# Performance work log

Hardware: AMD Instinct MI355X
Metric: run time of the kernel (lower is better)

## Reference

```python
import jax, jax.numpy as jnp
import numpy as np

CH = 128
GROUPS = 8
EPS = 1e-5

def group_norm(x, w, b):
    B, C, H, W = x.shape
    g = x.reshape(B, GROUPS, C // GROUPS, H, W)
    mean = g.mean(axis=(2, 3, 4), keepdims=True)
    var = g.var(axis=(2, 3, 4), keepdims=True)
    g = (g - mean) * jax.lax.rsqrt(var + EPS)
    g = g.reshape(B, C, H, W)
    return g * w[None, :, None, None] + b[None, :, None, None]

def setup_inputs() -> dict:
    key = jax.random.key(0)
    ks = jax.random.split(key, 7)
    C = CH
    x = jax.random.normal(ks[0], (8, C, 64, 64), dtype=jnp.float32)
    gn_w = jnp.ones((C,), dtype=jnp.float32)
    gn_b = jnp.zeros((C,), dtype=jnp.float32)
    s = 1.0 / np.sqrt(C)
    qkv_w = jax.random.normal(ks[1], (3 * C, C), dtype=jnp.float32) * s
    qkv_b = jax.random.normal(ks[2], (3 * C,), dtype=jnp.float32) * 0.01
    proj_w = jax.random.normal(ks[3], (C, C), dtype=jnp.float32) * s
    proj_b = jax.random.normal(ks[4], (C,), dtype=jnp.float32) * 0.01
    return {"x": x, "gn_w": gn_w, "gn_b": gn_b, "qkv_w": qkv_w,
            "qkv_b": qkv_b, "proj_w": proj_w, "proj_b": proj_b}

def reference(x, gn_w, gn_b, qkv_w, qkv_b, proj_w, proj_b):
    B, C, H, W = x.shape
    h = group_norm(x, gn_w, gn_b)
    # 1x1 conv == per-pixel matmul over channels
    qkv = jnp.einsum('bchw,oc->bohw', h, qkv_w) + qkv_b[None, :, None, None]
    q, k, v = jnp.split(qkv.reshape(B, 3 * C, H * W), 3, axis=1)  # each [B,C,N]
    scale = C ** (-0.5)
    attn = jax.nn.softmax(jnp.einsum('bci,bcj->bij', q * scale, k), axis=-1)
    out = jnp.einsum('bij,bcj->bci', attn, v).reshape(B, C, H, W)
    out = jnp.einsum('bchw,oc->bohw', out, proj_w) + proj_b[None, :, None, None]
    return x + out
```

## Files before the change

### kernel.cpp

```cpp
#include <hip/hip_runtime.h>
#include <stdint.h>


typedef __attribute__((ext_vector_type(8))) short short8;
typedef __attribute__((ext_vector_type(4))) float f32x4;
typedef __attribute__((ext_vector_type(16))) float f32x16;

#define MFMA_BF16(a, b, c) __builtin_amdgcn_mfma_f32_16x16x32_bf16((a), (b), (c), 0, 0, 0)
#define MFMA32(a, b, c) __builtin_amdgcn_mfma_f32_32x32x16_bf16((a), (b), (c), 0, 0, 0)
#define EXP2(x) __builtin_amdgcn_exp2f(x)

#define QSCALE 0.12751743f

__device__ __forceinline__ unsigned short f2bf(float f) {
    unsigned int u = __builtin_bit_cast(unsigned int, f);
    u += 0x7FFFu + ((u >> 16) & 1u);
    return (unsigned short)(u >> 16);
}
__device__ __forceinline__ float bf2f(unsigned int lo16) {
    return __builtin_bit_cast(float, lo16 << 16);
}
__device__ __forceinline__ short8 ldg8(const unsigned short* p) {
    return __builtin_bit_cast(short8, *(const uint4*)p);
}
__device__ __forceinline__ unsigned int cvtpk(float lo, float hi) {
    unsigned int r;
    asm("v_cvt_pk_bf16_f32 %0, %1, %2" : "=v"(r) : "v"(lo), "v"(hi));
    return r;
}
__device__ __forceinline__ void gload16(const void* g, void* l) {
    __builtin_amdgcn_global_load_lds(
        (__attribute__((address_space(1))) void*)g,
        (__attribute__((address_space(3))) void*)l, 16, 0, 0);
}

__global__ __launch_bounds__(256) void k_pre(const float* __restrict__ x,
                                             float* __restrict__ sums,
                                             const float* __restrict__ qkv_w,
                                             const float* __restrict__ proj_w,
                                             unsigned short* __restrict__ wq,
                                             unsigned short* __restrict__ wp) {
    if (blockIdx.x >= 1024) {
        int i = ((blockIdx.x - 1024) * 256 + threadIdx.x) * 4;
        const float* src; unsigned short* dst; int off;
        if (i < 49152) { src = qkv_w; dst = wq; off = i; }
        else           { src = proj_w; dst = wp; off = i - 49152; }
        float4 v = *(const float4*)(src + off);
        uint2 pk;
        pk.x = (unsigned int)f2bf(v.x) | ((unsigned int)f2bf(v.y) << 16);
        pk.y = (unsigned int)f2bf(v.z) | ((unsigned int)f2bf(v.w) << 16);
        *(uint2*)(dst + off) = pk;
        return;
    }
    int g     = blockIdx.x >> 4;
    int slice = blockIdx.x & 15;
    const float* p = x + (size_t)g * 65536 + slice * 4096;
    float s = 0.f, sq = 0.f;
#pragma unroll
    for (int i = 0; i < 4; ++i) {
        float4 v = *(const float4*)(p + threadIdx.x * 4 + i * 1024);
        s  += v.x + v.y + v.z + v.w;
        sq += v.x*v.x + v.y*v.y + v.z*v.z + v.w*v.w;
    }
#pragma unroll
    for (int m = 1; m < 64; m <<= 1) { s += __shfl_xor(s, m, 64); sq += __shfl_xor(sq, m, 64); }
    __shared__ float ss[4], ssq[4];
    int w = threadIdx.x >> 6;
    if ((threadIdx.x & 63) == 0) { ss[w] = s; ssq[w] = sq; }
    __syncthreads();
    if (threadIdx.x == 0) {
        sums[(g * 16 + slice) * 2]     = ss[0] + ss[1] + ss[2] + ss[3];
        sums[(g * 16 + slice) * 2 + 1] = ssq[0] + ssq[1] + ssq[2] + ssq[3];
    }
}

__global__ __launch_bounds__(256) void k_qkv(const float* __restrict__ x,
                                             const float* __restrict__ sums,
                                             const float* __restrict__ gn_w,
                                             const float* __restrict__ gn_b,
                                             const unsigned short* __restrict__ wq,
                                             const float* __restrict__ qkv_b,
                                             unsigned short* __restrict__ k_ws,
                                             unsigned short* __restrict__ v_ws) {
    __shared__ unsigned short h_lds[64][144];
    __shared__ float ms[8][2];
    const int tid  = threadIdx.x;
    const int b    = blockIdx.x >> 6;
    const int n0   = (blockIdx.x & 63) << 6;
    const int lane = tid & 63, wave = tid >> 6;
    const int l15  = lane & 15, q4 = lane >> 4;

    if (tid < 8) {
        float s = 0.f, q = 0.f;
        const float* sp = sums + (size_t)(b * 8 + tid) * 32;
#pragma unroll
        for (int i = 0; i < 16; ++i) { s += sp[i * 2]; q += sp[i * 2 + 1]; }
        float mean = s * (1.f / 65536.f);
        float var  = q * (1.f / 65536.f) - mean * mean;
        ms[tid][0] = mean;
        ms[tid][1] = rsqrtf(var + 1e-5f);
    }
    __syncthreads();

    {
        int cb = tid >> 4;
        int nn = (tid & 15) << 2;
#pragma unroll
        for (int k = 0; k < 8; ++k) {
            int c = cb + (k << 4);
            float4 v = *(const float4*)(x + ((size_t)(b * 128 + c) << 12) + n0 + nn);
            int g = c >> 4;
            float mean = ms[g][0];
            float rstd = ms[g][1];
            float ga = gn_w[c] * rstd;
            float be = gn_b[c] - mean * ga;
            h_lds[nn + 0][c] = f2bf(v.x * ga + be);
            h_lds[nn + 1][c] = f2bf(v.y * ga + be);
            h_lds[nn + 2][c] = f2bf(v.z * ga + be);
            h_lds[nn + 3][c] = f2bf(v.w * ga + be);
        }
    }
    __syncthreads();

    short8 bfrag[4][4];
#pragma unroll
    for (int nt = 0; nt < 4; ++nt)
#pragma unroll
        for (int ks = 0; ks < 4; ++ks)
            bfrag[nt][ks] = *(const short8*)&h_lds[nt * 16 + l15][ks * 32 + q4 * 8];
    __syncthreads();

    unsigned short* vstage = &h_lds[0][0];

#pragma unroll
    for (int ot = 0; ot < 4; ++ot) {
        int o0 = wave * 64 + ot * 16;
        short8 af[4];
#pragma unroll
        for (int ks = 0; ks < 4; ++ks)
            af[ks] = ldg8(wq + (size_t)(128 + o0 + l15) * 128 + ks * 32 + q4 * 8);

        if (o0 < 128) {
            float bias[4];
#pragma unroll
            for (int r = 0; r < 4; ++r) bias[r] = qkv_b[128 + o0 + q4 * 4 + r];
#pragma unroll
            for (int nt = 0; nt < 4; ++nt) {
                f32x4 acc = {0.f, 0.f, 0.f, 0.f};
#pragma unroll
                for (int ks = 0; ks < 4; ++ks)
                    acc = MFMA_BF16(af[ks], bfrag[nt][ks], acc);
                int n = n0 + nt * 16 + l15;
                unsigned int lo = (unsigned int)f2bf(acc[0] + bias[0]) |
                                  ((unsigned int)f2bf(acc[1] + bias[1]) << 16);
                unsigned int hi = (unsigned int)f2bf(acc[2] + bias[2]) |
                                  ((unsigned int)f2bf(acc[3] + bias[3]) << 16);
                uint2 pk; pk.x = lo; pk.y = hi;
                *(uint2*)&k_ws[((size_t)(b * 4096 + n) << 7) + o0 + q4 * 4] = pk;
            }
        } else {
            int c = o0 - 128 + l15;
            float vb = qkv_b[128 + o0 + l15];
#pragma unroll
            for (int nt = 0; nt < 4; ++nt) {
                f32x4 acc = {0.f, 0.f, 0.f, 0.f};
#pragma unroll
                for (int ks = 0; ks < 4; ++ks)
                    acc = MFMA_BF16(bfrag[nt][ks], af[ks], acc);
                unsigned int lo = (unsigned int)f2bf(acc[0] + vb) |
                                  ((unsigned int)f2bf(acc[1] + vb) << 16);
                unsigned int hi = (unsigned int)f2bf(acc[2] + vb) |
                                  ((unsigned int)f2bf(acc[3] + vb) << 16);
                uint2 pk; pk.x = lo; pk.y = hi;
                *(uint2*)&vstage[c * 72 + nt * 16 + q4 * 4] = pk;
            }
        }
    }
    __syncthreads();

    {
        int c = tid >> 1, hf = tid & 1;
        const unsigned short* src = vstage + c * 72 + hf * 32;
        unsigned short* dst = v_ws + ((size_t)(b * 128 + c) << 12) + n0 + hf * 32;
        uint4 a0 = *(const uint4*)(src + 0);
        uint4 a1 = *(const uint4*)(src + 8);
        uint4 a2 = *(const uint4*)(src + 16);
        uint4 a3 = *(const uint4*)(src + 24);
        *(uint4*)(dst + 0)  = a0;
        *(uint4*)(dst + 8)  = a1;
        *(uint4*)(dst + 16) = a2;
        *(uint4*)(dst + 24) = a3;
    }
}

__global__ __launch_bounds__(512, 2) void k_attn(const float* __restrict__ sums,
                                                 const float* __restrict__ gn_w,
                                                 const float* __restrict__ gn_b,
                                                 const unsigned short* __restrict__ wq,
                                                 const float* __restrict__ qkv_b,
                                                 const unsigned short* __restrict__ k_ws,
                                                 const unsigned short* __restrict__ v_ws,
                                                 const float* __restrict__ x,
                                                 const unsigned short* __restrict__ wp,
                                                 const float* __restrict__ proj_b,
                                                 float* __restrict__ out) {
    __shared__ unsigned short K0[64][128];
    __shared__ unsigned short K1[64][128];
    __shared__ unsigned short V0[128][64];
    __shared__ unsigned short V1[128][64];
    __shared__ unsigned short O_lds[128][136];
    __shared__ float Lp[256];
    __shared__ float ms[8][2];

    const int tid   = threadIdx.x;
    const int b     = blockIdx.x & 7;
    const int tile  = blockIdx.x >> 3;
    const int i0    = tile << 7;
    const int lane  = tid & 63, wave = tid >> 6;
    const int ih    = wave >> 1, jh = wave & 1;
    const int l31   = lane & 31, h = lane >> 5;
    const int irow  = ih * 32 + l31;

    if (tid < 8) {
        float s = 0.f, q = 0.f;
        const float* sp = sums + (size_t)(b * 8 + tid) * 32;
#pragma unroll
        for (int i = 0; i < 16; ++i) { s += sp[i * 2]; q += sp[i * 2 + 1]; }
        float mean = s * (1.f / 65536.f);
        float var  = q * (1.f / 65536.f) - mean * mean;
        ms[tid][0] = mean;
        ms[tid][1] = rsqrtf(var + 1e-5f);
    }
    __syncthreads();

    {
        int c = tid >> 2, qq = tid & 3;
        float mean = ms[c >> 4][0], rstd = ms[c >> 4][1];
        float ga = gn_w[c] * rstd;
        float be = gn_b[c] - mean * ga;
        const float* xp = x + ((size_t)(b * 128 + c) << 12) + i0 + qq * 32;
#pragma unroll
        for (int k = 0; k < 8; ++k) {
            float4 v = *(const float4*)(xp + k * 4);
            int il = qq * 32 + k * 4;
            O_lds[il + 0][c] = f2bf(v.x * ga + be);
            O_lds[il + 1][c] = f2bf(v.y * ga + be);
            O_lds[il + 2][c] = f2bf(v.z * ga + be);
            O_lds[il + 3][c] = f2bf(v.w * ga + be);
        }
    }
    __syncthreads();

    {
        const int l15 = lane & 15, q4 = lane >> 4;
        int o0q = wave * 16;
        short8 af[4];
#pragma unroll
        for (int ks = 0; ks < 4; ++ks)
            af[ks] = ldg8(wq + (size_t)(o0q + l15) * 128 + ks * 32 + q4 * 8);
        float qb[4];
#pragma unroll
        for (int r = 0; r < 4; ++r) qb[r] = qkv_b[o0q + q4 * 4 + r];
#pragma unroll
        for (int nt = 0; nt < 8; ++nt) {
            f32x4 qacc = {0.f, 0.f, 0.f, 0.f};
#pragma unroll
            for (int ks = 0; ks < 4; ++ks) {
                short8 bf = *(const short8*)&O_lds[nt * 16 + l15][ks * 32 + q4 * 8];
                qacc = MFMA_BF16(af[ks], bf, qacc);
            }
            unsigned int lo = (unsigned int)f2bf((qacc[0] + qb[0]) * QSCALE) |
                              ((unsigned int)f2bf((qacc[1] + qb[1]) * QSCALE) << 16);
            unsigned int hi = (unsigned int)f2bf((qacc[2] + qb[2]) * QSCALE) |
                              ((unsigned int)f2bf((qacc[3] + qb[3]) * QSCALE) << 16);
            uint2 pk; pk.x = lo; pk.y = hi;
            unsigned short* qrow = (nt < 4) ? &K0[nt * 16 + l15][0]
                                            : &K1[(nt - 4) * 16 + l15][0];
            *(uint2*)(qrow + o0q + q4 * 4) = pk;
        }
    }
    __syncthreads();

    short8 qf[8];
    {
        const unsigned short* qrow = (ih < 2) ? &K0[irow][0] : &K1[irow - 64][0];
#pragma unroll
        for (int ks = 0; ks < 8; ++ks)
            qf[ks] = *(const short8*)(qrow + ks * 16 + h * 8);
    }
    __syncthreads();

    f32x16 acc[4];
#pragma unroll
    for (int ct = 0; ct < 4; ++ct)
#pragma unroll
        for (int e = 0; e < 16; ++e) acc[ct][e] = 0.f;
    float l_run = 0.f;

    const unsigned short* kbase = k_ws + ((size_t)b << 19);
    int ksrc[2];
#pragma unroll
    for (int q = 0; q < 2; ++q) {
        int c   = q * 512 + tid;
        int row = c >> 4;
        ksrc[q] = row * 16 + ((c & 15) ^ (row & 15));
    }
    const unsigned short* vlane = v_ws + ((size_t)b << 19) +
        ((size_t)(tid >> 3) << 12) +
        ((((tid & 7) ^ ((tid >> 3) & 7) ^ wave)) << 3);

#define STAGE(T, KD, VD)                                                              \
  do {                                                                                \
    _Pragma("unroll")                                                                 \
    for (int q = 0; q < 2; ++q)                                                       \
      gload16(kbase + (size_t)(T) * 8192 + ksrc[q] * 8,                               \
              (char*)(&KD[0][0]) + q * 8192 + wave * 1024);                           \
    _Pragma("unroll")                                                                 \
    for (int q = 0; q < 2; ++q)                                                       \
      gload16(vlane + (size_t)q * 262144 + (T) * 64,                                  \
              (char*)(&VD[0][0]) + q * 8192 + wave * 1024);                           \
  } while (0)

#define BAR_A()                                                                       \
  do {                                                                                \
    asm volatile("s_waitcnt vmcnt(0)" ::: "memory");                                  \
    __builtin_amdgcn_s_barrier();                                                     \
    __builtin_amdgcn_sched_barrier(0);                                                \
  } while (0)

    const int krow = jh * 32 + l31;
    const int ksw  = l31 & 15;
    const int vk   = (l31 & 7) ^ (l31 >> 3);

    STAGE(0, K0, V0);

#define ATTN_ITER(IT, KR, VR, KP, VP)                                                 \
  do {                                                                                \
    BAR_A();                          \
    if ((IT) < 63) STAGE((IT) + 1, KP, VP);           \
    f32x16 s;        \
    _Pragma("unroll")                                                                 \
    for (int e = 0; e < 16; ++e) s[e] = 0.f;                                          \
    _Pragma("unroll")                                                                 \
    for (int ks = 0; ks < 8; ++ks) {                                                  \
      short8 kf = *(const short8*)&KR[krow][((ks * 2 + h) ^ ksw) << 3];               \
      s = MFMA32(kf, qf[ks], s);                                                      \
    }                                                                                 \
    float pvv[16];                         \
    _Pragma("unroll")                                                                 \
    for (int e = 0; e < 16; ++e) pvv[e] = EXP2(fminf(s[e], 30.f));                    \
    l_run += (((pvv[0] + pvv[1]) + (pvv[2] + pvv[3])) +                               \
              ((pvv[4] + pvv[5]) + (pvv[6] + pvv[7]))) +                              \
             (((pvv[8] + pvv[9]) + (pvv[10] + pvv[11])) +                             \
              ((pvv[12] + pvv[13]) + (pvv[14] + pvv[15])));                           \
    short8 paf[2];     \
    _Pragma("unroll")                                                                 \
    for (int ks = 0; ks < 2; ++ks) {                                                  \
      const float* pp = pvv + ks * 8;                                                 \
      unsigned int Wa = cvtpk(pp[0], pp[1]);                                          \
      unsigned int Wc = cvtpk(pp[2], pp[3]);                                          \
      unsigned int Wb = cvtpk(pp[4], pp[5]);                                          \
      unsigned int Wd = cvtpk(pp[6], pp[7]);                                          \
      auto r1 = __builtin_amdgcn_permlane32_swap(Wa, Wb, false, false);               \
      auto r2 = __builtin_amdgcn_permlane32_swap(Wc, Wd, false, false);               \
      uint4 aw; aw.x = r1[0]; aw.y = r2[0]; aw.z = r1[1]; aw.w = r2[1];               \
      paf[ks] = __builtin_bit_cast(short8, aw);              \
    }                                                                                 \
    _Pragma("unroll")                                                                 \
    for (int ks = 0; ks < 2; ++ks)                                                    \
      _Pragma("unroll")                                                               \
      for (int ct = 0; ct < 4; ++ct) {                                                \
        short8 vf = *(const short8*)&VR[ct * 32 + l31]                                \
            [((jh * 4 + ks * 2 + h) ^ vk ^ ((ct & 1) << 2)) << 3];                    \
        acc[ct] = MFMA32(paf[ks], vf, acc[ct]);                                       \
      }                                                                               \
  } while (0)

    for (int ib = 0; ib < 32; ++ib) {
        int it = ib * 2;
        ATTN_ITER(it,     K0, V0, K1, V1);
        ATTN_ITER(it + 1, K1, V1, K0, V0);
    }
#undef ATTN_ITER
#undef STAGE
#undef BAR_A

    __syncthreads();
    float l2 = l_run + __shfl_xor(l_run, 32);
    if (h == 0) Lp[jh * 128 + irow] = l2;
    float* ObLow  = (ih < 2) ? (float*)&K0[0][0] : (float*)&K1[0][0];
    float* ObHigh = (ih < 2) ? (float*)&V0[0][0] : (float*)&V1[0][0];
    const int vbase = (ih & 1) * 32;
    if (jh) {
#pragma unroll
        for (int cc = 0; cc < 2; ++cc)
#pragma unroll
            for (int r = 0; r < 16; ++r) {
                int il = (r & 3) + ((r >> 2) << 3) + (h << 2);
                ObLow[(vbase + il) * 64 + cc * 32 + l31] = (cc == 0) ? acc[0][r] : acc[1][r];
            }
    } else {
#pragma unroll
        for (int cc = 0; cc < 2; ++cc)
#pragma unroll
            for (int r = 0; r < 16; ++r) {
                int il = (r & 3) + ((r >> 2) << 3) + (h << 2);
                ObHigh[(vbase + il) * 64 + cc * 32 + l31] = (cc == 0) ? acc[2][r] : acc[3][r];
            }
    }
    __syncthreads();
    {
        float rl[16];
#pragma unroll
        for (int r = 0; r < 16; ++r) {
            int il = (r & 3) + ((r >> 2) << 3) + (h << 2);
            rl[r] = 1.0f / (Lp[ih * 32 + il] + Lp[128 + ih * 32 + il]);
        }
        if (jh) {
#pragma unroll
            for (int cc = 0; cc < 2; ++cc)
#pragma unroll
                for (int r = 0; r < 16; ++r) {
                    int il = (r & 3) + ((r >> 2) << 3) + (h << 2);
                    float own = (cc == 0) ? acc[2][r] : acc[3][r];
                    float v = own + ObHigh[(vbase + il) * 64 + cc * 32 + l31];
                    O_lds[ih * 32 + il][64 + cc * 32 + l31] = f2bf(v * rl[r]);
                }
        } else {
#pragma unroll
            for (int cc = 0; cc < 2; ++cc)
#pragma unroll
                for (int r = 0; r < 16; ++r) {
                    int il = (r & 3) + ((r >> 2) << 3) + (h << 2);
                    float own = (cc == 0) ? acc[0][r] : acc[1][r];
                    float v = own + ObLow[(vbase + il) * 64 + cc * 32 + l31];
                    O_lds[ih * 32 + il][cc * 32 + l31] = f2bf(v * rl[r]);
                }
        }
    }
    __syncthreads();

    {
        const int l15 = lane & 15, q4 = lane >> 4;
        int o0 = wave * 16;
        short8 af[4];
#pragma unroll
        for (int ks = 0; ks < 4; ++ks)
            af[ks] = ldg8(wp + (size_t)(o0 + l15) * 128 + ks * 32 + q4 * 8);
        float pb[4];
#pragma unroll
        for (int r = 0; r < 4; ++r) pb[r] = proj_b[o0 + q4 * 4 + r];

#pragma unroll
        for (int nt = 0; nt < 8; ++nt) {
            f32x4 pacc = {0.f, 0.f, 0.f, 0.f};
#pragma unroll
            for (int ks = 0; ks < 4; ++ks) {
                short8 bf = *(const short8*)&O_lds[nt * 16 + l15][ks * 32 + q4 * 8];
                pacc = MFMA_BF16(af[ks], bf, pacc);
            }
#pragma unroll
            for (int r = 0; r < 4; ++r) {
                size_t idx = ((size_t)(b * 128 + o0 + q4 * 4 + r) << 12) +
                             i0 + nt * 16 + l15;
                out[idx] = x[idx] + pacc[r] + pb[r];
            }
        }
    }
}

extern "C" void kernel_launch(void* const* d_in, const int* in_sizes, int n_in,
                              void* d_out, int out_size, void* d_ws, size_t ws_size,
                              hipStream_t stream) {
    const float* x      = (const float*)d_in[0];
    const float* gn_w   = (const float*)d_in[1];
    const float* gn_b   = (const float*)d_in[2];
    const float* qkv_w  = (const float*)d_in[3];
    const float* qkv_b  = (const float*)d_in[4];
    const float* proj_w = (const float*)d_in[5];
    const float* proj_b = (const float*)d_in[6];
    float* out = (float*)d_out;

    char* ws = (char*)d_ws;
    float* sums           = (float*)ws;
    unsigned short* wq    = (unsigned short*)(ws + 16384);
    unsigned short* wp    = (unsigned short*)(ws + 16384 + 98304);
    unsigned short* k_ws  = (unsigned short*)(ws + ((size_t)1 << 20));
    unsigned short* v_ws  = (unsigned short*)(ws + ((size_t)9 << 20));

    k_pre<<<1088, 256, 0, stream>>>(x, sums, qkv_w, proj_w, wq, wp);
    k_qkv<<<512, 256, 0, stream>>>(x, sums, gn_w, gn_b, wq, qkv_b, k_ws, v_ws);
    k_attn<<<256, 512, 0, stream>>>(sums, gn_w, gn_b, wq, qkv_b, k_ws, v_ws,
                                    x, wp, proj_b, out);
}
```

Before: 175.4 us.

## Fuse all three stages into one cooperative kernel with grid-wide syncs

Merges the stats/weight-conversion, QKV projection and attention kernels into a single cooperative kernel of 256 blocks that uses grid.sync between phases. Each block computes partial group-norm sums for its own 128-pixel tile, then after a grid barrier normalizes, projects Q into LDS and writes its K/V tile to the workspace. A second grid barrier precedes attention. This removes two kernel launches and the redundant re-read of x for the stats, at the cost of grid-wide barriers and the occupancy limits that cooperative launch imposes.

```diff
diff --git a/kernel.cpp b/kernel.cpp
--- a/kernel.cpp
+++ b/kernel.cpp
@@ -1,6 +1,9 @@
 #include <hip/hip_runtime.h>
+#include <hip/hip_cooperative_groups.h>
 #include <stdint.h>
 
+
+namespace cg = cooperative_groups;
 
 typedef __attribute__((ext_vector_type(8))) short short8;
 typedef __attribute__((ext_vector_type(4))) float f32x4;
@@ -17,9 +20,6 @@
     u += 0x7FFFu + ((u >> 16) & 1u);
     return (unsigned short)(u >> 16);
 }
-__device__ __forceinline__ float bf2f(unsigned int lo16) {
-    return __builtin_bit_cast(float, lo16 << 16);
-}
 __device__ __forceinline__ short8 ldg8(const unsigned short* p) {
     return __builtin_bit_cast(short8, *(const uint4*)p);
 }
@@ -34,67 +34,74 @@
         (__attribute__((address_space(3))) void*)l, 16, 0, 0);
 }
 
-__global__ __launch_bounds__(256) void k_pre(const float* __restrict__ x,
-                                             float* __restrict__ sums,
-                                             const float* __restrict__ qkv_w,
-                                             const float* __restrict__ proj_w,
-                                             unsigned short* __restrict__ wq,
-                                             unsigned short* __restrict__ wp) {
-    if (blockIdx.x >= 1024) {
-        int i = ((blockIdx.x - 1024) * 256 + threadIdx.x) * 4;
+__global__ __launch_bounds__(512, 2) void k_fused(const float* __restrict__ x,
+                                                  float* __restrict__ sums,
+                                                  const float* __restrict__ qkv_w_raw,
+                                                  const float* __restrict__ proj_w_raw,
+                                                  unsigned short* __restrict__ wq,
+                                                  unsigned short* __restrict__ wp,
+                                                  const float* __restrict__ gn_w,
+                                                  const float* __restrict__ gn_b,
+                                                  const float* __restrict__ qkv_b,
+                                                  unsigned short* __restrict__ k_ws,
+                                                  unsigned short* __restrict__ v_ws,
+                                                  const float* __restrict__ proj_b,
+                                                  float* __restrict__ out) {
+    __shared__ unsigned short K0[64][128];
+    __shared__ unsigned short K1[64][128];
+    __shared__ unsigned short V0[128][64];
+    __shared__ unsigned short V1[128][64];
+    __shared__ unsigned short O_lds[128][136];
+    __shared__ float Lp[256];
+    __shared__ float ms[8][2];
+
+    const int tid   = threadIdx.x;
+    const int b     = blockIdx.x & 7;
+    const int tile  = blockIdx.x >> 3;
+    const int i0    = tile << 7;
+    const int lane  = tid & 63, wave = tid >> 6;
+    const int ih    = wave >> 1, jh = wave & 1;
+    const int l31   = lane & 31, h = lane >> 5;
+    const int irow  = ih * 32 + l31;
+    const int l15   = lane & 15, q4 = lane >> 4;
+
+    cg::grid_group grid = cg::this_grid();
+
+    if (tid < 64) {
+        int i = (blockIdx.x * 64 + tid) * 4;
         const float* src; unsigned short* dst; int off;
-        if (i < 49152) { src = qkv_w; dst = wq; off = i; }
-        else           { src = proj_w; dst = wp; off = i - 49152; }
+        if (i < 49152) { src = qkv_w_raw; dst = wq; off = i; }
+        else           { src = proj_w_raw; dst = wp; off = i - 49152; }
         float4 v = *(const float4*)(src + off);
         uint2 pk;
         pk.x = (unsigned int)f2bf(v.x) | ((unsigned int)f2bf(v.y) << 16);
         pk.y = (unsigned int)f2bf(v.z) | ((unsigned int)f2bf(v.w) << 16);
         *(uint2*)(dst + off) = pk;
-        return;
-    }
-    int g     = blockIdx.x >> 4;
-    int slice = blockIdx.x & 15;
-    const float* p = x + (size_t)g * 65536 + slice * 4096;
-    float s = 0.f, sq = 0.f;
-#pragma unroll
-    for (int i = 0; i < 4; ++i) {
-        float4 v = *(const float4*)(p + threadIdx.x * 4 + i * 1024);
-        s  += v.x + v.y + v.z + v.w;
-        sq += v.x*v.x + v.y*v.y + v.z*v.z + v.w*v.w;
-    }
-#pragma unroll
-    for (int m = 1; m < 64; m <<= 1) { s += __shfl_xor(s, m, 64); sq += __shfl_xor(sq, m, 64); }
-    __shared__ float ss[4], ssq[4];
-    int w = threadIdx.x >> 6;
-    if ((threadIdx.x & 63) == 0) { ss[w] = s; ssq[w] = sq; }
-    __syncthreads();
-    if (threadIdx.x == 0) {
-        sums[(g * 16 + slice) * 2]     = ss[0] + ss[1] + ss[2] + ss[3];
-        sums[(g * 16 + slice) * 2 + 1] = ssq[0] + ssq[1] + ssq[2] + ssq[3];
-    }
-}
-
-__global__ __launch_bounds__(256) void k_qkv(const float* __restrict__ x,
-                                             const float* __restrict__ sums,
-                                             const float* __restrict__ gn_w,
-                                             const float* __restrict__ gn_b,
-                                             const unsigned short* __restrict__ wq,
-                                             const float* __restrict__ qkv_b,
-                                             unsigned short* __restrict__ k_ws,
-                                             unsigned short* __restrict__ v_ws) {
-    __shared__ unsigned short h_lds[64][144];
-    __shared__ float ms[8][2];
-    const int tid  = threadIdx.x;
-    const int b    = blockIdx.x >> 6;
-    const int n0   = (blockIdx.x & 63) << 6;
-    const int lane = tid & 63, wave = tid >> 6;
-    const int l15  = lane & 15, q4 = lane >> 4;
+    }
+    {
+        int c = tid >> 2, qq = tid & 3;
+        const float* xp = x + ((size_t)(b * 128 + c) << 12) + i0 + qq * 32;
+        float s = 0.f, sq = 0.f;
+#pragma unroll
+        for (int k = 0; k < 8; ++k) {
+            float4 v = *(const float4*)(xp + k * 4);
+            s  += v.x + v.y + v.z + v.w;
+            sq += v.x*v.x + v.y*v.y + v.z*v.z + v.w*v.w;
+        }
+#pragma unroll
+        for (int m = 1; m < 64; m <<= 1) { s += __shfl_xor(s, m, 64); sq += __shfl_xor(sq, m, 64); }
+        if (lane == 0) {
+            sums[((b * 8 + wave) * 32 + tile) * 2]     = s;
+            sums[((b * 8 + wave) * 32 + tile) * 2 + 1] = sq;
+        }
+    }
+    grid.sync();
 
     if (tid < 8) {
         float s = 0.f, q = 0.f;
-        const float* sp = sums + (size_t)(b * 8 + tid) * 32;
-#pragma unroll
-        for (int i = 0; i < 16; ++i) { s += sp[i * 2]; q += sp[i * 2 + 1]; }
+        const float* sp = sums + (size_t)((b * 8 + tid) * 32) * 2;
+#pragma unroll
+        for (int i = 0; i < 32; ++i) { s += sp[i * 2]; q += sp[i * 2 + 1]; }
         float mean = s * (1.f / 65536.f);
         float var  = q * (1.f / 65536.f) - mean * mean;
         ms[tid][0] = mean;
@@ -103,85 +110,109 @@
     __syncthreads();
 
     {
-        int cb = tid >> 4;
-        int nn = (tid & 15) << 2;
+        int c = tid >> 2, qq = tid & 3;
+        float mean = ms[c >> 4][0], rstd = ms[c >> 4][1];
+        float ga = gn_w[c] * rstd;
+        float be = gn_b[c] - mean * ga;
+        const float* xp = x + ((size_t)(b * 128 + c) << 12) + i0 + qq * 32;
 #pragma unroll
         for (int k = 0; k < 8; ++k) {
-            int c = cb + (k << 4);
-            float4 v = *(const float4*)(x + ((size_t)(b * 128 + c) << 12) + n0 + nn);
-            int g = c >> 4;
-            float mean = ms[g][0];
-            float rstd = ms[g][1];
-            float ga = gn_w[c] * rstd;
-            float be = gn_b[c] - mean * ga;
-            h_lds[nn + 0][c] = f2bf(v.x * ga + be);
-            h_lds[nn + 1][c] = f2bf(v.y * ga + be);
-            h_lds[nn + 2][c] = f2bf(v.z * ga + be);
-            h_lds[nn + 3][c] = f2bf(v.w * ga + be);
-        }
-    }
-    __syncthreads();
-
-    short8 bfrag[4][4];
-#pragma unroll
-    for (int nt = 0; nt < 4; ++nt)
+            float4 v = *(const float4*)(xp + k * 4);
+            int il = qq * 32 + k * 4;
+            O_lds[il + 0][c] = f2bf(v.x * ga + be);
+            O_lds[il + 1][c] = f2bf(v.y * ga + be);
+            O_lds[il + 2][c] = f2bf(v.z * ga + be);
+            O_lds[il + 3][c] = f2bf(v.w * ga + be);
+        }
+    }
+    __syncthreads();
+
+    {
+        int o0q = wave * 16;
+        short8 af[4];
 #pragma unroll
         for (int ks = 0; ks < 4; ++ks)
-            bfrag[nt][ks] = *(const short8*)&h_lds[nt * 16 + l15][ks * 32 + q4 * 8];
-    __syncthreads();
-
-    unsigned short* vstage = &h_lds[0][0];
-
-#pragma unroll
-    for (int ot = 0; ot < 4; ++ot) {
-        int o0 = wave * 64 + ot * 16;
+            af[ks] = ldg8(wq + (size_t)(o0q + l15) * 128 + ks * 32 + q4 * 8);
+        float qb[4];
+#pragma unroll
+        for (int r = 0; r < 4; ++r) qb[r] = qkv_b[o0q + q4 * 4 + r];
+#pragma unroll
+        for (int nt = 0; nt < 8; ++nt) {
+            f32x4 qacc = {0.f, 0.f, 0.f, 0.f};
+#pragma unroll
+            for (int ks = 0; ks < 4; ++ks) {
+                short8 bf = *(const short8*)&O_lds[nt * 16 + l15][ks * 32 + q4 * 8];
+                qacc = MFMA_BF16(af[ks], bf, qacc);
+            }
+            unsigned int lo = (unsigned int)f2bf((qacc[0] + qb[0]) * QSCALE) |
+                              ((unsigned int)f2bf((qacc[1] + qb[1]) * QSCALE) << 16);
+            unsigned int hi = (unsigned int)f2bf((qacc[2] + qb[2]) * QSCALE) |
+                              ((unsigned int)f2bf((qacc[3] + qb[3]) * QSCALE) << 16);
+            uint2 pk; pk.x = lo; pk.y = hi;
+            unsigned short* qrow = (nt < 4) ? &K0[nt * 16 + l15][0]
+                                            : &K1[(nt - 4) * 16 + l15][0];
+            *(uint2*)(qrow + o0q + q4 * 4) = pk;
+        }
+    }
+    {
+        int o0 = wave * 16;
         short8 af[4];
 #pragma unroll
         for (int ks = 0; ks < 4; ++ks)
             af[ks] = ldg8(wq + (size_t)(128 + o0 + l15) * 128 + ks * 32 + q4 * 8);
-
-        if (o0 < 128) {
-            float bias[4];
-#pragma unroll
-            for (int r = 0; r < 4; ++r) bias[r] = qkv_b[128 + o0 + q4 * 4 + r];
-#pragma unroll
-            for (int nt = 0; nt < 4; ++nt) {
-                f32x4 acc = {0.f, 0.f, 0.f, 0.f};
-#pragma unroll
-                for (int ks = 0; ks < 4; ++ks)
-                    acc = MFMA_BF16(af[ks], bfrag[nt][ks], acc);
-                int n = n0 + nt * 16 + l15;
-                unsigned int lo = (unsigned int)f2bf(acc[0] + bias[0]) |
-                                  ((unsigned int)f2bf(acc[1] + bias[1]) << 16);
-                unsigned int hi = (unsigned int)f2bf(acc[2] + bias[2]) |
-                                  ((unsigned int)f2bf(acc[3] + bias[3]) << 16);
-                uint2 pk; pk.x = lo; pk.y = hi;
-                *(uint2*)&k_ws[((size_t)(b * 4096 + n) << 7) + o0 + q4 * 4] = pk;
-            }
-        } else {
-            int c = o0 - 128 + l15;
-            float vb = qkv_b[128 + o0 + l15];
-#pragma unroll
-            for (int nt = 0; nt < 4; ++nt) {
-                f32x4 acc = {0.f, 0.f, 0.f, 0.f};
-#pragma unroll
-                for (int ks = 0; ks < 4; ++ks)
-                    acc = MFMA_BF16(bfrag[nt][ks], af[ks], acc);
-                unsigned int lo = (unsigned int)f2bf(acc[0] + vb) |
-                                  ((unsigned int)f2bf(acc[1] + vb) << 16);
-                unsigned int hi = (unsigned int)f2bf(acc[2] + vb) |
-                                  ((unsigned int)f2bf(acc[3] + vb) << 16);
-                uint2 pk; pk.x = lo; pk.y = hi;
-                *(uint2*)&vstage[c * 72 + nt * 16 + q4 * 4] = pk;
-            }
-        }
-    }
-    __syncthreads();
-
-    {
-        int c = tid >> 1, hf = tid & 1;
-        const unsigned short* src = vstage + c * 72 + hf * 32;
-        unsigned short* dst = v_ws + ((size_t)(b * 128 + c) << 12) + n0 + hf * 32;
+        float bias[4];
+#pragma unroll
+        for (int r = 0; r < 4; ++r) bias[r] = qkv_b[128 + o0 + q4 * 4 + r];
+#pragma unroll
+        for (int nt = 0; nt < 8; ++nt) {
+            f32x4 acc = {0.f, 0.f, 0.f, 0.f};
+#pragma unroll
+            for (int ks = 0; ks < 4; ++ks) {
+                short8 bf = *(const short8*)&O_lds[nt * 16 + l15][ks * 32 + q4 * 8];
+                acc = MFMA_BF16(af[ks], bf, acc);
+            }
+            int n = i0 + nt * 16 + l15;
+            unsigned int lo = (unsigned int)f2bf(acc[0] + bias[0]) |
+                              ((unsigned int)f2bf(acc[1] + bias[1]) << 16);
+            unsigned int hi = (unsigned int)f2bf(acc[2] + bias[2]) |
+                              ((unsigned int)f2bf(acc[3] + bias[3]) << 16);
+            uint2 pk; pk.x = lo; pk.y = hi;
+            *(uint2*)&k_ws[((size_t)(b * 4096 + n) << 7) + o0 + q4 * 4] = pk;
+        }
+    }
+    {
+        int c = wave * 16 + l15;
+        short8 af[4];
+#pragma unroll
+        for (int ks = 0; ks < 4; ++ks)
+            af[ks] = ldg8(wq + (size_t)(256 + wave * 16 + l15) * 128 + ks * 32 + q4 * 8);
+        float vb = qkv_b[256 + wave * 16 + l15];
+        unsigned short* vrow = ((wave < 4) ? (unsigned short*)&V0[0][0]
+                                           : (unsigned short*)&V1[0][0]) + (c & 63) * 128;
+#pragma unroll
+        for (int nt = 0; nt < 8; ++nt) {
+            f32x4 acc = {0.f, 0.f, 0.f, 0.f};
+#pragma unroll
+            for (int ks = 0; ks < 4; ++ks) {
+                short8 bf = *(const short8*)&O_lds[nt * 16 + l15][ks * 32 + q4 * 8];
+                acc = MFMA_BF16(bf, af[ks], acc);
+            }
+            unsigned int lo = (unsigned int)f2bf(acc[0] + vb) |
+                              ((unsigned int)f2bf(acc[1] + vb) << 16);
+            unsigned int hi = (unsigned int)f2bf(acc[2] + vb) |
+                              ((unsigned int)f2bf(acc[3] + vb) << 16);
+            uint2 pk; pk.x = lo; pk.y = hi;
+            *(uint2*)&vrow[nt * 16 + q4 * 4] = pk;
+        }
+    }
+    __syncthreads();
+
+    {
+        int c = tid >> 2, qq = tid & 3;
+        const unsigned short* src = ((c < 64) ? (const unsigned short*)&V0[0][0]
+                                              : (const unsigned short*)&V1[0][0]) +
+                                    (c & 63) * 128 + qq * 32;
+        unsigned short* dst = v_ws + ((size_t)(b * 128 + c) << 12) + i0 + qq * 32;
         uint4 a0 = *(const uint4*)(src + 0);
         uint4 a1 = *(const uint4*)(src + 8);
         uint4 a2 = *(const uint4*)(src + 16);
@@ -191,96 +222,6 @@
         *(uint4*)(dst + 16) = a2;
         *(uint4*)(dst + 24) = a3;
     }
-}
-
-__global__ __launch_bounds__(512, 2) void k_attn(const float* __restrict__ sums,
-                                                 const float* __restrict__ gn_w,
-                                                 const float* __restrict__ gn_b,
-                                                 const unsigned short* __restrict__ wq,
-                                                 const float* __restrict__ qkv_b,
-                                                 const unsigned short* __restrict__ k_ws,
-                                                 const unsigned short* __restrict__ v_ws,
-                                                 const float* __restrict__ x,
-                                                 const unsigned short* __restrict__ wp,
-                                                 const float* __restrict__ proj_b,
-                                                 float* __restrict__ out) {
-    __shared__ unsigned short K0[64][128];
-    __shared__ unsigned short K1[64][128];
-    __shared__ unsigned short V0[128][64];
-    __shared__ unsigned short V1[128][64];
-    __shared__ unsigned short O_lds[128][136];
-    __shared__ float Lp[256];
-    __shared__ float ms[8][2];
-
-    const int tid   = threadIdx.x;
-    const int b     = blockIdx.x & 7;
-    const int tile  = blockIdx.x >> 3;
-    const int i0    = tile << 7;
-    const int lane  = tid & 63, wave = tid >> 6;
-    const int ih    = wave >> 1, jh = wave & 1;
-    const int l31   = lane & 31, h = lane >> 5;
-    const int irow  = ih * 32 + l31;
-
-    if (tid < 8) {
-        float s = 0.f, q = 0.f;
-        const float* sp = sums + (size_t)(b * 8 + tid) * 32;
-#pragma unroll
-        for (int i = 0; i < 16; ++i) { s += sp[i * 2]; q += sp[i * 2 + 1]; }
-        float mean = s * (1.f / 65536.f);
-        float var  = q * (1.f / 65536.f) - mean * mean;
-        ms[tid][0] = mean;
-        ms[tid][1] = rsqrtf(var + 1e-5f);
-    }
-    __syncthreads();
-
-    {
-        int c = tid >> 2, qq = tid & 3;
-        float mean = ms[c >> 4][0], rstd = ms[c >> 4][1];
-        float ga = gn_w[c] * rstd;
-        float be = gn_b[c] - mean * ga;
-        const float* xp = x + ((size_t)(b * 128 + c) << 12) + i0 + qq * 32;
-#pragma unroll
-        for (int k = 0; k < 8; ++k) {
-            float4 v = *(const float4*)(xp + k * 4);
-            int il = qq * 32 + k * 4;
-            O_lds[il + 0][c] = f2bf(v.x * ga + be);
-            O_lds[il + 1][c] = f2bf(v.y * ga + be);
-            O_lds[il + 2][c] = f2bf(v.z * ga + be);
-            O_lds[il + 3][c] = f2bf(v.w * ga + be);
-        }
-    }
-    __syncthreads();
-
-    {
-        const int l15 = lane & 15, q4 = lane >> 4;
-        int o0q = wave * 16;
-        short8 af[4];
-#pragma unroll
-        for (int ks = 0; ks < 4; ++ks)
-            af[ks] = ldg8(wq + (size_t)(o0q + l15) * 128 + ks * 32 + q4 * 8);
-        float qb[4];
-#pragma unroll
-        for (int r = 0; r < 4; ++r) qb[r] = qkv_b[o0q + q4 * 4 + r];
-#pragma unroll
-        for (int nt = 0; nt < 8; ++nt) {
-            f32x4 qacc = {0.f, 0.f, 0.f, 0.f};
-#pragma unroll
-            for (int ks = 0; ks < 4; ++ks) {
-                short8 bf = *(const short8*)&O_lds[nt * 16 + l15][ks * 32 + q4 * 8];
-                qacc = MFMA_BF16(af[ks], bf, qacc);
-            }
-            unsigned int lo = (unsigned int)f2bf((qacc[0] + qb[0]) * QSCALE) |
-                              ((unsigned int)f2bf((qacc[1] + qb[1]) * QSCALE) << 16);
-            unsigned int hi = (unsigned int)f2bf((qacc[2] + qb[2]) * QSCALE) |
-                              ((unsigned int)f2bf((qacc[3] + qb[3]) * QSCALE) << 16);
-            uint2 pk; pk.x = lo; pk.y = hi;
-            unsigned short* qrow = (nt < 4) ? &K0[nt * 16 + l15][0]
-                                            : &K1[(nt - 4) * 16 + l15][0];
-            *(uint2*)(qrow + o0q + q4 * 4) = pk;
-        }
-    }
-    __syncthreads();
-
     short8 qf[8];
     {
         const unsigned short* qrow = (ih < 2) ? &K0[irow][0] : &K1[irow - 64][0];
@@ -289,6 +230,7 @@
             qf[ks] = *(const short8*)(qrow + ks * 16 + h * 8);
     }
     __syncthreads();
+    grid.sync();
 
     f32x16 acc[4];
 #pragma unroll
@@ -336,9 +278,9 @@
 
 #define ATTN_ITER(IT, KR, VR, KP, VP)                                                 \
   do {                                                                                \
-    BAR_A();                          \
-    if ((IT) < 63) STAGE((IT) + 1, KP, VP);           \
-    f32x16 s;        \
+    BAR_A();                                                                          \
+    if ((IT) < 63) STAGE((IT) + 1, KP, VP);                                           \
+    f32x16 s;                                                                         \
     _Pragma("unroll")                                                                 \
     for (int e = 0; e < 16; ++e) s[e] = 0.f;                                          \
     _Pragma("unroll")                                                                 \
@@ -346,14 +288,14 @@
       short8 kf = *(const short8*)&KR[krow][((ks * 2 + h) ^ ksw) << 3];               \
       s = MFMA32(kf, qf[ks], s);                                                      \
     }                                                                                 \
-    float pvv[16];                         \
+    float pvv[16];                                                                    \
     _Pragma("unroll")                                                                 \
     for (int e = 0; e < 16; ++e) pvv[e] = EXP2(fminf(s[e], 30.f));                    \
     l_run += (((pvv[0] + pvv[1]) + (pvv[2] + pvv[3])) +                               \
               ((pvv[4] + pvv[5]) + (pvv[6] + pvv[7]))) +                              \
              (((pvv[8] + pvv[9]) + (pvv[10] + pvv[11])) +                             \
               ((pvv[12] + pvv[13]) + (pvv[14] + pvv[15])));                           \
-    short8 paf[2];     \
+    short8 paf[2];                                                                    \
     _Pragma("unroll")                                                                 \
     for (int ks = 0; ks < 2; ++ks) {                                                  \
       const float* pp = pvv + ks * 8;                                                 \
@@ -364,7 +306,7 @@
       auto r1 = __builtin_amdgcn_permlane32_swap(Wa, Wb, false, false);               \
       auto r2 = __builtin_amdgcn_permlane32_swap(Wc, Wd, false, false);               \
       uint4 aw; aw.x = r1[0]; aw.y = r2[0]; aw.z = r1[1]; aw.w = r2[1];               \
-      paf[ks] = __builtin_bit_cast(short8, aw);              \
+      paf[ks] = __builtin_bit_cast(short8, aw);                                       \
     }                                                                                 \
     _Pragma("unroll")                                                                 \
     for (int ks = 0; ks < 2; ++ks)                                                    \
@@ -441,7 +383,6 @@
     __syncthreads();
 
     {
-        const int l15 = lane & 15, q4 = lane >> 4;
         int o0 = wave * 16;
         short8 af[4];
 #pragma unroll
@@ -488,8 +429,10 @@
     unsigned short* k_ws  = (unsigned short*)(ws + ((size_t)1 << 20));
     unsigned short* v_ws  = (unsigned short*)(ws + ((size_t)9 << 20));
 
-    k_pre<<<1088, 256, 0, stream>>>(x, sums, qkv_w, proj_w, wq, wp);
-    k_qkv<<<512, 256, 0, stream>>>(x, sums, gn_w, gn_b, wq, qkv_b, k_ws, v_ws);
-    k_attn<<<256, 512, 0, stream>>>(sums, gn_w, gn_b, wq, qkv_b, k_ws, v_ws,
-                                    x, wp, proj_b, out);
-}
+    void* args[] = { (void*)&x, (void*)&sums, (void*)&qkv_w, (void*)&proj_w,
+                     (void*)&wq, (void*)&wp, (void*)&gn_w, (void*)&gn_b,
+                     (void*)&qkv_b, (void*)&k_ws, (void*)&v_ws,
+                     (void*)&proj_b, (void*)&out };
+    hipLaunchCooperativeKernel((void*)k_fused, dim3(256), dim3(512),
+                               args, 0, stream);
+}
```

After: 238.8 us. +36.2%, slower.
